# Performance work log

Hardware: AMD Instinct MI355X
Metric: run time of the kernel (lower is better)

## Reference

```python
import jax, jax.numpy as jnp
import numpy as np

T, B, IN, H = 256, 128, 512, 1024


def setup_inputs() -> dict:
    key = jax.random.key(0)
    ks = jax.random.split(key, 13)
    s = 1.0 / float(np.sqrt(H))  # torch LSTMCell init: U(-1/sqrt(H), 1/sqrt(H))
    u = lambda k, shp: jax.random.uniform(k, shp, jnp.float32, -s, s)
    return {
        "x": jax.random.normal(ks[0], (T, B, IN), jnp.float32),
        "h0_fwd": jax.random.normal(ks[1], (B, H), jnp.float32),
        "c0_fwd": jax.random.normal(ks[2], (B, H), jnp.float32),
        "h0_rev": jax.random.normal(ks[3], (B, H), jnp.float32),
        "c0_rev": jax.random.normal(ks[4], (B, H), jnp.float32),
        "W_ih_f": u(ks[5], (4 * H, IN)),
        "W_hh_f": u(ks[6], (4 * H, H)),
        "b_ih_f": u(ks[7], (4 * H,)),
        "b_hh_f": u(ks[8], (4 * H,)),
        "W_ih_r": u(ks[9], (4 * H, IN)),
        "W_hh_r": u(ks[10], (4 * H, H)),
        "b_ih_r": u(ks[11], (4 * H,)),
        "b_hh_r": u(ks[12], (4 * H,)),
    }


def _lstm(x, h0, c0, Wih, Whh, bih, bhh, reverse):
    # Precompute the input projection for all timesteps in one big GEMM.
    xp = jnp.einsum('tbi,gi->tbg', x, Wih) + bih + bhh  # [T, B, 4H]

    def step(carry, xg):
        h, c = carry
        gates = xg + h @ Whh.T  # [B, 4H]
        i, f, g, o = jnp.split(gates, 4, axis=-1)  # torch gate order: i, f, g, o
        c = jax.nn.sigmoid(f) * c + jax.nn.sigmoid(i) * jnp.tanh(g)
        h = jax.nn.sigmoid(o) * jnp.tanh(c)
        return (h, c), h

    # reverse=True scans backward in time but emits outputs in original order,
    # exactly matching ReverseLSTMLayer's reverse-process-then-reverse-outputs.
    (h, c), ys = jax.lax.scan(step, (h0, c0), xp, reverse=reverse)
    return ys, h, c


def reference(x, h0_fwd, c0_fwd, h0_rev, c0_rev,
              W_ih_f, W_hh_f, b_ih_f, b_hh_f,
              W_ih_r, W_hh_r, b_ih_r, b_hh_r):
    yf, hf, cf = _lstm(x, h0_fwd, c0_fwd, W_ih_f, W_hh_f, b_ih_f, b_hh_f, False)
    yr, hr, cr = _lstm(x, h0_rev, c0_rev, W_ih_r, W_hh_r, b_ih_r, b_hh_r, True)
    out = jnp.concatenate([yf, yr], axis=-1)  # [T, B, 2H]
    # Faithful to the original's `hidden, cell = output_states` quirk:
    # `hidden` is the forward direction's (h, c) pair stacked,
    # `cell` is the reverse direction's (h, c) pair stacked.
    hidden = jnp.stack([hf, cf])  # [2, B, H]
    cell = jnp.stack([hr, cr])    # [2, B, H]
    return out, (hidden, cell)
```

## Files before the change

kernel.cpp:

```cpp
#include <hip/hip_runtime.h>
#include <hip/hip_bf16.h>

typedef unsigned short u16;
typedef __attribute__((ext_vector_type(8))) short bf16x8;
typedef __attribute__((ext_vector_type(8))) u16   u16x8;
typedef __attribute__((ext_vector_type(4))) float f32x4;

#define T_STEPS 256
#define BATCH   128
#define INDIM   512
#define HDIM    1024
#define GDIM    4096
#define KTOT    1536

#define OFF_XBF   ((size_t)0)
#define XBF_BYTES ((size_t)T_STEPS * BATCH * INDIM * 2)
#define OFF_BM    (OFF_XBF + XBF_BYTES)
#define BM_BYTES  ((size_t)2 * GDIM * KTOT * 2)
#define OFF_BIAS  (OFF_BM + BM_BYTES)
#define BIAS_BYTES ((size_t)2 * GDIM * 4)
#define OFF_CNT   (OFF_BIAS + BIAS_BYTES)
#define OFF_ROLL  (OFF_CNT + 8192)
#define ROLL_BYTES ((size_t)(T_STEPS + 1) * 2 * BATCH * HDIM * 2)
#define WS_NEED   (OFF_ROLL + ROLL_BYTES)

__device__ __forceinline__ u16 f2b(float f) {
  __hip_bfloat16 h = __float2bfloat16(f);
  return *reinterpret_cast<u16*>(&h);
}

__device__ __forceinline__ void glds16(const void* g, void* l) {
  __builtin_amdgcn_global_load_lds(
      (const __attribute__((address_space(1))) unsigned int*)g,
      (__attribute__((address_space(3))) unsigned int*)l, 16, 0, 0);
}

__global__ void k_cast_x(const float* __restrict__ x, u16* __restrict__ xb) {
  size_t i = ((size_t)blockIdx.x * 256 + threadIdx.x) * 8;
  f32x4 a = *reinterpret_cast<const f32x4*>(x + i);
  f32x4 b = *reinterpret_cast<const f32x4*>(x + i + 4);
  u16x8 u;
  u[0] = f2b(a[0]); u[1] = f2b(a[1]); u[2] = f2b(a[2]); u[3] = f2b(a[3]);
  u[4] = f2b(b[0]); u[5] = f2b(b[1]); u[6] = f2b(b[2]); u[7] = f2b(b[3]);
  *reinterpret_cast<u16x8*>(xb + i) = u;
}

__global__ void k_build_b(const float* __restrict__ Whh_f, const float* __restrict__ Wih_f,
                          const float* __restrict__ Whh_r, const float* __restrict__ Wih_r,
                          u16* __restrict__ Bm) {
  int blk = blockIdx.x;
  int dir = blk >> 6, jt = blk & 63;
  const float* Whh = dir ? Whh_r : Whh_f;
  const float* Wih = dir ? Wih_r : Wih_f;
  u16* dst = Bm + (size_t)blk * 64 * KTOT;
  for (int c = 0; c < 64; c++) {
    int G = (c >> 4) * HDIM + jt * 16 + (c & 15);
    for (int k = threadIdx.x; k < KTOT; k += 256) {
      float v = (k < HDIM) ? Whh[(size_t)G * HDIM + k] : Wih[(size_t)G * INDIM + (k - HDIM)];
      dst[c * KTOT + k] = f2b(v);
    }
  }
}

__global__ void k_init(const float* __restrict__ h0f, const float* __restrict__ h0r,
                       const float* __restrict__ bihf, const float* __restrict__ bhhf,
                       const float* __restrict__ bihr, const float* __restrict__ bhhr,
                       u16* __restrict__ hroll, float* __restrict__ bias,
                       unsigned* __restrict__ flags) {
  int i = blockIdx.x * 256 + threadIdx.x;
  if (i < 2 * BATCH * HDIM) {
    int dir = i / (BATCH * HDIM);
    int rem = i - dir * BATCH * HDIM;
    int r = rem / HDIM, c = rem - r * HDIM;
    const float* h0 = dir ? h0r : h0f;
    char* hb = (char*)hroll;
    *(u16*)(hb + ((size_t)dir * BATCH + r) * 2048 + ((2 * c) ^ ((r & 7) << 4))) =
        f2b(h0[rem]);
  }
  if (i < 2 * GDIM) {
    int dir = i / GDIM, g = i - dir * GDIM;
    bias[i] = dir ? (bihr[g] + bhhr[g]) : (bihf[g] + bhhf[g]);
  }
  if (i < 512) flags[i] = 0;
}

__global__ __launch_bounds__(512, 2) void k_lstm(
    const u16* __restrict__ xb, const u16* __restrict__ Bm,
    u16* __restrict__ hroll,
    const float* __restrict__ bias, unsigned* __restrict__ flags,
    const float* __restrict__ c0f, const float* __restrict__ c0r,
    float* __restrict__ out) {
  __shared__ float ldsf[8 * 64 * 68];
  char* ldsc = reinterpret_cast<char*>(ldsf);

  __builtin_amdgcn_fence(__ATOMIC_ACQUIRE, "agent");

  const int wg   = blockIdx.x;
  const int xcd  = wg & 7, local = wg >> 3;
  const int grp  = xcd >> 1;
  const int dir  = grp >> 1, mt = grp & 1;
  const int jt   = ((xcd & 1) << 5) | local;
  const int tid = threadIdx.x;
  const int w = tid >> 6, lane = tid & 63;
  const int kk = (lane >> 4) * 8;
  const int ar = lane & 15;

  const u16* bsrc = Bm + (size_t)(dir * 64 + jt) * 64 * KTOT;
  bf16x8 bh[4][4];
#pragma unroll
  for (int ks = 0; ks < 4; ks++)
#pragma unroll
    for (int ni = 0; ni < 4; ni++)
      bh[ks][ni] = *reinterpret_cast<const bf16x8*>(
          bsrc + (size_t)(ni * 16 + ar) * KTOT + 128 * w + 32 * ks + kk);

  const int rrow = tid >> 3;
  const int cp   = tid & 7;
  const int jl0  = 2 * cp;
  const int row0 = mt * 64 + rrow;
  const int jg0  = jt * 16 + jl0;
  const float* c0 = dir ? c0r : c0f;
  float2 cc = *reinterpret_cast<const float2*>(c0 + (size_t)row0 * HDIM + jg0);
  float cst0 = cc.x, cst1 = cc.y;
  const float2 b_i = *reinterpret_cast<const float2*>(bias + dir * GDIM + 0 * HDIM + jg0);
  const float2 b_f = *reinterpret_cast<const float2*>(bias + dir * GDIM + 1 * HDIM + jg0);
  const float2 b_g = *reinterpret_cast<const float2*>(bias + dir * GDIM + 2 * HDIM + jg0);
  const float2 b_o = *reinterpret_cast<const float2*>(bias + dir * GDIM + 3 * HDIM + jg0);

  const unsigned* fpA = flags + grp * 64 + lane;

#pragma unroll 1
  for (int s = 0; s < T_STEPS; s++) {
    const int t = dir ? (T_STEPS - 1 - s) : s;

    bf16x8 axm[2][4], bxn[2][4];
    {
      const u16* xsrc = xb + ((size_t)t * BATCH + mt * 64) * INDIM;
#pragma unroll
      for (int ks = 0; ks < 2; ks++) {
#pragma unroll
        for (int mi = 0; mi < 4; mi++)
          axm[ks][mi] = *reinterpret_cast<const bf16x8*>(
              xsrc + (size_t)(16 * mi + ar) * INDIM + 64 * w + 32 * ks + kk);
#pragma unroll
        for (int ni = 0; ni < 4; ni++)
          bxn[ks][ni] = *reinterpret_cast<const bf16x8*>(
              bsrc + (size_t)(ni * 16 + ar) * KTOT + HDIM + 64 * w + 32 * ks + kk);
      }
    }

    if (s > 0) {
      while (true) {
        unsigned f = __hip_atomic_load(fpA, __ATOMIC_RELAXED, __HIP_MEMORY_SCOPE_AGENT);
        if (__all((int)(f >= (unsigned)s))) break;
        __builtin_amdgcn_s_sleep(1);
      }
      __builtin_amdgcn_sched_barrier(0);
    }

    {
      const char* hRd = (const char*)(hroll + ((size_t)s * 2 + dir) * BATCH * HDIM
                                            + (size_t)mt * 64 * HDIM);
      unsigned off = (unsigned)w * 1024 + (unsigned)(lane * 16);
#pragma unroll
      for (int i = 0; i < 16; i++)
        glds16(hRd + off + i * 8192, ldsc + off + i * 8192);
    }

    f32x4 acc[4][4];
#pragma unroll
    for (int mi = 0; mi < 4; mi++)
#pragma unroll
      for (int ni = 0; ni < 4; ni++) acc[mi][ni] = f32x4{0.f, 0.f, 0.f, 0.f};
#pragma unroll
    for (int ks = 0; ks < 2; ks++)
#pragma unroll
      for (int mi = 0; mi < 4; mi++)
#pragma unroll
        for (int ni = 0; ni < 4; ni++)
          acc[mi][ni] = __builtin_amdgcn_mfma_f32_16x16x32_bf16(axm[ks][mi], bxn[ks][ni], acc[mi][ni], 0, 0, 0);

    __syncthreads();

#pragma unroll
    for (int ks = 0; ks < 4; ks++)
#pragma unroll
      for (int mi = 0; mi < 4; mi++) {
        unsigned row = 16 * mi + ar;
        unsigned cb = (128 * w + 32 * ks + kk) * 2;
        bf16x8 af = *reinterpret_cast<const bf16x8*>(
            ldsc + row * 2048 + (cb ^ ((row & 7) << 4)));
#pragma unroll
        for (int ni = 0; ni < 4; ni++)
          acc[mi][ni] = __builtin_amdgcn_mfma_f32_16x16x32_bf16(af, bh[ks][ni], acc[mi][ni], 0, 0, 0);
      }
    __syncthreads();

    {
      float* pw = ldsf + w * (64 * 68);
#pragma unroll
      for (int mi = 0; mi < 4; mi++)
#pragma unroll
        for (int ni = 0; ni < 4; ni++)
          *reinterpret_cast<f32x4*>(pw + (ni * 16 + ar) * 68 + mi * 16 + (lane >> 4) * 4) = acc[mi][ni];
    }
    __syncthreads();

    float h0v, h1v;
    {
      float gi0 = b_i.x, gi1 = b_i.y, gf0 = b_f.x, gf1 = b_f.y;
      float gg0 = b_g.x, gg1 = b_g.y, go0 = b_o.x, go1 = b_o.y;
#pragma unroll
      for (int ww = 0; ww < 8; ww++) {
        const float* p = ldsf + ww * (64 * 68);
        gi0 += p[(0 * 16 + jl0) * 68 + rrow]; gi1 += p[(0 * 16 + jl0 + 1) * 68 + rrow];
        gf0 += p[(1 * 16 + jl0) * 68 + rrow]; gf1 += p[(1 * 16 + jl0 + 1) * 68 + rrow];
        gg0 += p[(2 * 16 + jl0) * 68 + rrow]; gg1 += p[(2 * 16 + jl0 + 1) * 68 + rrow];
        go0 += p[(3 * 16 + jl0) * 68 + rrow]; go1 += p[(3 * 16 + jl0 + 1) * 68 + rrow];
      }
      float i0 = 1.f / (1.f + __expf(-gi0)), i1 = 1.f / (1.f + __expf(-gi1));
      float f0 = 1.f / (1.f + __expf(-gf0)), f1 = 1.f / (1.f + __expf(-gf1));
      float g0 = tanhf(gg0), g1 = tanhf(gg1);
      float o0 = 1.f / (1.f + __expf(-go0)), o1 = 1.f / (1.f + __expf(-go1));
      cst0 = f0 * cst0 + i0 * g0;
      cst1 = f1 * cst1 + i1 * g1;
      h0v = o0 * tanhf(cst0);
      h1v = o1 * tanhf(cst1);

      unsigned hp = (unsigned)f2b(h0v) | ((unsigned)f2b(h1v) << 16);
      char* hb = (char*)(hroll + ((size_t)(s + 1) * 2 + dir) * BATCH * HDIM);
      __hip_atomic_store(
          (unsigned*)(hb + (size_t)row0 * 2048 + ((2 * jg0) ^ ((row0 & 7) << 4))),
          hp, __ATOMIC_RELAXED, __HIP_MEMORY_SCOPE_AGENT);
    }

    asm volatile("s_waitcnt vmcnt(0)" ::: "memory");
    __syncthreads();
    if (tid == 0)
      __hip_atomic_store(flags + grp * 64 + jt, (unsigned)(s + 1),
                         __ATOMIC_RELAXED, __HIP_MEMORY_SCOPE_AGENT);

    {
      float2 yv; yv.x = h0v; yv.y = h1v;
      *reinterpret_cast<float2*>(out + ((size_t)t * BATCH + row0) * (2 * HDIM)
                                     + (size_t)dir * HDIM + jg0) = yv;
      if (s == T_STEPS - 1) {
        size_t hid = (size_t)T_STEPS * BATCH * 2 * HDIM;
        size_t base2 = hid + (size_t)dir * 2 * BATCH * HDIM;
        *reinterpret_cast<float2*>(out + base2 + (size_t)row0 * HDIM + jg0) = yv;
        float2 cv; cv.x = cst0; cv.y = cst1;
        *reinterpret_cast<float2*>(out + base2 + (size_t)BATCH * HDIM
                                       + (size_t)row0 * HDIM + jg0) = cv;
      }
    }
  }
}

extern "C" void kernel_launch(void* const* d_in, const int* in_sizes, int n_in,
                              void* d_out, int out_size, void* d_ws, size_t ws_size,
                              hipStream_t stream) {
  const float* x     = (const float*)d_in[0];
  const float* h0f   = (const float*)d_in[1];
  const float* c0f   = (const float*)d_in[2];
  const float* h0r   = (const float*)d_in[3];
  const float* c0r   = (const float*)d_in[4];
  const float* Wih_f = (const float*)d_in[5];
  const float* Whh_f = (const float*)d_in[6];
  const float* bih_f = (const float*)d_in[7];
  const float* bhh_f = (const float*)d_in[8];
  const float* Wih_r = (const float*)d_in[9];
  const float* Whh_r = (const float*)d_in[10];
  const float* bih_r = (const float*)d_in[11];
  const float* bhh_r = (const float*)d_in[12];
  float* out = (float*)d_out;
  char* ws = (char*)d_ws;

  if (ws_size < WS_NEED) return;

  u16* xbf        = (u16*)(ws + OFF_XBF);
  u16* Bm         = (u16*)(ws + OFF_BM);
  float* bias     = (float*)(ws + OFF_BIAS);
  unsigned* flags = (unsigned*)(ws + OFF_CNT);
  u16* hroll      = (u16*)(ws + OFF_ROLL);

  k_cast_x<<<8192, 256, 0, stream>>>(x, xbf);
  k_build_b<<<128, 256, 0, stream>>>(Whh_f, Wih_f, Whh_r, Wih_r, Bm);
  k_init<<<1024, 256, 0, stream>>>(h0f, h0r, bih_f, bhh_f, bih_r, bhh_r,
                                   hroll, bias, flags);
  k_lstm<<<256, 512, 0, stream>>>(xbf, Bm, hroll, bias, flags, c0f, c0r, out);
}
```

Baseline: 2.038 ms.

## Retile persistent LSTM to 32-row x 128-gate tiles with pre-swizzled x

Each workgroup now owns 32 batch rows by 32 hidden units (128 gate columns) instead of 64 rows by 16 units. Waves split K into four quarters and N into two halves, keeping all recurrent and input weights in registers. This halves the per-step h tile copied into LDS and shrinks the cross-wave reduction from 8 to 4 partials. x is pre-swizzled into MFMA fragment order so each lane does contiguous loads, and the redundant per-step reload of input weights is gone. The trade-off is much higher register pressure from holding 48 weight fragments per lane, plus a changed flag/XCD grouping that may alter which workgroups wait on each other.

```diff
diff --git a/kernel.cpp b/kernel.cpp
--- a/kernel.cpp
+++ b/kernel.cpp
@@ -35,26 +35,37 @@
       (__attribute__((address_space(3))) unsigned int*)l, 16, 0, 0);
 }
 
-__global__ void k_cast_x(const float* __restrict__ x, u16* __restrict__ xb) {
-  size_t i = ((size_t)blockIdx.x * 256 + threadIdx.x) * 8;
-  f32x4 a = *reinterpret_cast<const f32x4*>(x + i);
-  f32x4 b = *reinterpret_cast<const f32x4*>(x + i + 4);
+__global__ void k_cast_x(const float* __restrict__ x, u16* __restrict__ xs) {
+  int i = blockIdx.x * 256 + threadIdx.x;
+  int t   = i >> 13;
+  int r13 = i & 8191;
+  int row = r13 >> 6;
+  int c0  = (r13 & 63) * 8;
+  int q = row >> 5, rloc = row & 31;
+  int mi = rloc >> 4, ar = rloc & 15;
+  int kq = c0 >> 7, kr = c0 & 127;
+  int ks = kr >> 5, h4 = (kr & 31) >> 3;
+  int lane = h4 * 16 + ar;
+  const float* src = x + ((size_t)t * BATCH + row) * INDIM + c0;
+  f32x4 a = *reinterpret_cast<const f32x4*>(src);
+  f32x4 b = *reinterpret_cast<const f32x4*>(src + 4);
   u16x8 u;
   u[0] = f2b(a[0]); u[1] = f2b(a[1]); u[2] = f2b(a[2]); u[3] = f2b(a[3]);
   u[4] = f2b(b[0]); u[5] = f2b(b[1]); u[6] = f2b(b[2]); u[7] = f2b(b[3]);
-  *reinterpret_cast<u16x8*>(xb + i) = u;
+  size_t dst = ((((((size_t)t * 4 + q) * 4 + kq) * 4 + ks) * 2 + mi) * 64 + lane) * 8;
+  *reinterpret_cast<u16x8*>(xs + dst) = u;
 }
 
 __global__ void k_build_b(const float* __restrict__ Whh_f, const float* __restrict__ Wih_f,
                           const float* __restrict__ Whh_r, const float* __restrict__ Wih_r,
                           u16* __restrict__ Bm) {
   int blk = blockIdx.x;
-  int dir = blk >> 6, jt = blk & 63;
+  int dir = blk >> 5, jt = blk & 31;
   const float* Whh = dir ? Whh_r : Whh_f;
   const float* Wih = dir ? Wih_r : Wih_f;
-  u16* dst = Bm + (size_t)blk * 64 * KTOT;
-  for (int c = 0; c < 64; c++) {
-    int G = (c >> 4) * HDIM + jt * 16 + (c & 15);
+  u16* dst = Bm + (size_t)blk * 128 * KTOT;
+  for (int c = 0; c < 128; c++) {
+    int G = (c >> 5) * HDIM + jt * 32 + (c & 31);
     for (int k = threadIdx.x; k < KTOT; k += 256) {
       float v = (k < HDIM) ? Whh[(size_t)G * HDIM + k] : Wih[(size_t)G * INDIM + (k - HDIM)];
       dst[c * KTOT + k] = f2b(v);
@@ -85,40 +96,46 @@
 }
 
 __global__ __launch_bounds__(512, 2) void k_lstm(
-    const u16* __restrict__ xb, const u16* __restrict__ Bm,
+    const u16* __restrict__ xs, const u16* __restrict__ Bm,
     u16* __restrict__ hroll,
     const float* __restrict__ bias, unsigned* __restrict__ flags,
     const float* __restrict__ c0f, const float* __restrict__ c0r,
     float* __restrict__ out) {
-  __shared__ float ldsf[8 * 64 * 68];
+  __shared__ float ldsf[34816];
   char* ldsc = reinterpret_cast<char*>(ldsf);
+  float* ldsP = ldsf + 16384;
 
   __builtin_amdgcn_fence(__ATOMIC_ACQUIRE, "agent");
 
   const int wg   = blockIdx.x;
-  const int xcd  = wg & 7, local = wg >> 3;
-  const int grp  = xcd >> 1;
-  const int dir  = grp >> 1, mt = grp & 1;
-  const int jt   = ((xcd & 1) << 5) | local;
-  const int tid = threadIdx.x;
+  const int grp  = wg & 7;
+  const int dir  = grp >> 2, q = grp & 3;
+  const int jt32 = wg >> 3;
+  const int tid  = threadIdx.x;
   const int w = tid >> 6, lane = tid & 63;
-  const int kk = (lane >> 4) * 8;
+  const int kq = w >> 1, nh = w & 1;
+  const int h4 = lane >> 4, kk = h4 * 8;
   const int ar = lane & 15;
 
-  const u16* bsrc = Bm + (size_t)(dir * 64 + jt) * 64 * KTOT;
-  bf16x8 bh[4][4];
-#pragma unroll
-  for (int ks = 0; ks < 4; ks++)
+  const u16* bsrc = Bm + (size_t)(dir * 32 + jt32) * 128 * KTOT;
+  bf16x8 bh[8][4], bx[4][4];
+#pragma unroll
+  for (int ks = 0; ks < 8; ks++)
 #pragma unroll
     for (int ni = 0; ni < 4; ni++)
       bh[ks][ni] = *reinterpret_cast<const bf16x8*>(
-          bsrc + (size_t)(ni * 16 + ar) * KTOT + 128 * w + 32 * ks + kk);
-
-  const int rrow = tid >> 3;
-  const int cp   = tid & 7;
-  const int jl0  = 2 * cp;
-  const int row0 = mt * 64 + rrow;
-  const int jg0  = jt * 16 + jl0;
+          bsrc + (size_t)(nh * 64 + ni * 16 + ar) * KTOT + 256 * kq + 32 * ks + kk);
+#pragma unroll
+  for (int ks = 0; ks < 4; ks++)
+#pragma unroll
+    for (int ni = 0; ni < 4; ni++)
+      bx[ks][ni] = *reinterpret_cast<const bf16x8*>(
+          bsrc + (size_t)(nh * 64 + ni * 16 + ar) * KTOT + HDIM + 128 * kq + 32 * ks + kk);
+
+  const int rrow = tid & 31;
+  const int jl0  = 2 * (tid >> 5);
+  const int row0 = q * 32 + rrow;
+  const int jg0  = jt32 * 32 + jl0;
   const float* c0 = dir ? c0r : c0f;
   float2 cc = *reinterpret_cast<const float2*>(c0 + (size_t)row0 * HDIM + jg0);
   float cst0 = cc.x, cst1 = cc.y;
@@ -127,26 +144,21 @@
   const float2 b_g = *reinterpret_cast<const float2*>(bias + dir * GDIM + 2 * HDIM + jg0);
   const float2 b_o = *reinterpret_cast<const float2*>(bias + dir * GDIM + 3 * HDIM + jg0);
 
-  const unsigned* fpA = flags + grp * 64 + lane;
+  const unsigned* fpA = flags + grp * 32 + (lane & 31);
 
 #pragma unroll 1
   for (int s = 0; s < T_STEPS; s++) {
     const int t = dir ? (T_STEPS - 1 - s) : s;
 
-    bf16x8 axm[2][4], bxn[2][4];
-    {
-      const u16* xsrc = xb + ((size_t)t * BATCH + mt * 64) * INDIM;
-#pragma unroll
-      for (int ks = 0; ks < 2; ks++) {
-#pragma unroll
-        for (int mi = 0; mi < 4; mi++)
-          axm[ks][mi] = *reinterpret_cast<const bf16x8*>(
-              xsrc + (size_t)(16 * mi + ar) * INDIM + 64 * w + 32 * ks + kk);
-#pragma unroll
-        for (int ni = 0; ni < 4; ni++)
-          bxn[ks][ni] = *reinterpret_cast<const bf16x8*>(
-              bsrc + (size_t)(ni * 16 + ar) * KTOT + HDIM + 64 * w + 32 * ks + kk);
-      }
+    bf16x8 ax[4][2];
+    {
+      const u16* xb = xs + ((((size_t)t * 4 + q) * 4 + kq) * 4) * 2 * 512;
+#pragma unroll
+      for (int ks = 0; ks < 4; ks++)
+#pragma unroll
+        for (int mi = 0; mi < 2; mi++)
+          ax[ks][mi] = *reinterpret_cast<const bf16x8*>(
+              xb + ((size_t)(ks * 2 + mi) * 64 + lane) * 8);
     }
 
     if (s > 0) {
@@ -159,50 +171,56 @@
     }
 
     {
-      const char* hRd = (const char*)(hroll + ((size_t)s * 2 + dir) * BATCH * HDIM
-                                            + (size_t)mt * 64 * HDIM);
-      unsigned off = (unsigned)w * 1024 + (unsigned)(lane * 16);
-#pragma unroll
-      for (int i = 0; i < 16; i++)
+      const char* hRd = (const char*)hroll + ((size_t)s * 2 + dir) * (BATCH * 2048)
+                        + (size_t)q * 32 * 2048;
+      unsigned off = (unsigned)tid * 16;
+#pragma unroll
+      for (int i = 0; i < 8; i++)
         glds16(hRd + off + i * 8192, ldsc + off + i * 8192);
     }
-
-    f32x4 acc[4][4];
-#pragma unroll
-    for (int mi = 0; mi < 4; mi++)
+    __builtin_amdgcn_sched_barrier(0);
+
+    f32x4 acc[2][4];
+#pragma unroll
+    for (int mi = 0; mi < 2; mi++)
 #pragma unroll
       for (int ni = 0; ni < 4; ni++) acc[mi][ni] = f32x4{0.f, 0.f, 0.f, 0.f};
 #pragma unroll
-    for (int ks = 0; ks < 2; ks++)
-#pragma unroll
-      for (int mi = 0; mi < 4; mi++)
+    for (int ks = 0; ks < 4; ks++)
+#pragma unroll
+      for (int mi = 0; mi < 2; mi++)
 #pragma unroll
         for (int ni = 0; ni < 4; ni++)
-          acc[mi][ni] = __builtin_amdgcn_mfma_f32_16x16x32_bf16(axm[ks][mi], bxn[ks][ni], acc[mi][ni], 0, 0, 0);
+          acc[mi][ni] = __builtin_amdgcn_mfma_f32_16x16x32_bf16(ax[ks][mi], bx[ks][ni], acc[mi][ni], 0, 0, 0);
 
     __syncthreads();
 
 #pragma unroll
-    for (int ks = 0; ks < 4; ks++)
-#pragma unroll
-      for (int mi = 0; mi < 4; mi++) {
+    for (int ks = 0; ks < 8; ks++) {
+      bf16x8 af[2];
+#pragma unroll
+      for (int mi = 0; mi < 2; mi++) {
         unsigned row = 16 * mi + ar;
-        unsigned cb = (128 * w + 32 * ks + kk) * 2;
-        bf16x8 af = *reinterpret_cast<const bf16x8*>(
+        unsigned cb = (256 * kq + 32 * ks + kk) * 2;
+        af[mi] = *reinterpret_cast<const bf16x8*>(
             ldsc + row * 2048 + (cb ^ ((row & 7) << 4)));
+      }
+#pragma unroll
+      for (int mi = 0; mi < 2; mi++)
 #pragma unroll
         for (int ni = 0; ni < 4; ni++)
-          acc[mi][ni] = __builtin_amdgcn_mfma_f32_16x16x32_bf16(af, bh[ks][ni], acc[mi][ni], 0, 0, 0);
-      }
-    __syncthreads();
-
-    {
-      float* pw = ldsf + w * (64 * 68);
-#pragma unroll
-      for (int mi = 0; mi < 4; mi++)
-#pragma unroll
-        for (int ni = 0; ni < 4; ni++)
-          *reinterpret_cast<f32x4*>(pw + (ni * 16 + ar) * 68 + mi * 16 + (lane >> 4) * 4) = acc[mi][ni];
+          acc[mi][ni] = __builtin_amdgcn_mfma_f32_16x16x32_bf16(af[mi], bh[ks][ni], acc[mi][ni], 0, 0, 0);
+    }
+
+    {
+      float* pw = ldsP + kq * (128 * 36);
+#pragma unroll
+      for (int mi = 0; mi < 2; mi++)
+#pragma unroll
+        for (int ni = 0; ni < 4; ni++) {
+          int col = nh * 64 + ni * 16 + ar;
+          *reinterpret_cast<f32x4*>(pw + col * 36 + mi * 16 + h4 * 4) = acc[mi][ni];
+        }
     }
     __syncthreads();
 
@@ -211,12 +229,12 @@
       float gi0 = b_i.x, gi1 = b_i.y, gf0 = b_f.x, gf1 = b_f.y;
       float gg0 = b_g.x, gg1 = b_g.y, go0 = b_o.x, go1 = b_o.y;
 #pragma unroll
-      for (int ww = 0; ww < 8; ww++) {
-        const float* p = ldsf + ww * (64 * 68);
-        gi0 += p[(0 * 16 + jl0) * 68 + rrow]; gi1 += p[(0 * 16 + jl0 + 1) * 68 + rrow];
-        gf0 += p[(1 * 16 + jl0) * 68 + rrow]; gf1 += p[(1 * 16 + jl0 + 1) * 68 + rrow];
-        gg0 += p[(2 * 16 + jl0) * 68 + rrow]; gg1 += p[(2 * 16 + jl0 + 1) * 68 + rrow];
-        go0 += p[(3 * 16 + jl0) * 68 + rrow]; go1 += p[(3 * 16 + jl0 + 1) * 68 + rrow];
+      for (int k4 = 0; k4 < 4; k4++) {
+        const float* p = ldsP + k4 * (128 * 36);
+        gi0 += p[(0 * 32 + jl0) * 36 + rrow]; gi1 += p[(0 * 32 + jl0 + 1) * 36 + rrow];
+        gf0 += p[(1 * 32 + jl0) * 36 + rrow]; gf1 += p[(1 * 32 + jl0 + 1) * 36 + rrow];
+        gg0 += p[(2 * 32 + jl0) * 36 + rrow]; gg1 += p[(2 * 32 + jl0 + 1) * 36 + rrow];
+        go0 += p[(3 * 32 + jl0) * 36 + rrow]; go1 += p[(3 * 32 + jl0 + 1) * 36 + rrow];
       }
       float i0 = 1.f / (1.f + __expf(-gi0)), i1 = 1.f / (1.f + __expf(-gi1));
       float f0 = 1.f / (1.f + __expf(-gf0)), f1 = 1.f / (1.f + __expf(-gf1));
@@ -228,7 +246,7 @@
       h1v = o1 * tanhf(cst1);
 
       unsigned hp = (unsigned)f2b(h0v) | ((unsigned)f2b(h1v) << 16);
-      char* hb = (char*)(hroll + ((size_t)(s + 1) * 2 + dir) * BATCH * HDIM);
+      char* hb = (char*)hroll + ((size_t)(s + 1) * 2 + dir) * (BATCH * 2048);
       __hip_atomic_store(
           (unsigned*)(hb + (size_t)row0 * 2048 + ((2 * jg0) ^ ((row0 & 7) << 4))),
           hp, __ATOMIC_RELAXED, __HIP_MEMORY_SCOPE_AGENT);
@@ -237,7 +255,7 @@
     asm volatile("s_waitcnt vmcnt(0)" ::: "memory");
     __syncthreads();
     if (tid == 0)
-      __hip_atomic_store(flags + grp * 64 + jt, (unsigned)(s + 1),
+      __hip_atomic_store(flags + grp * 32 + jt32, (unsigned)(s + 1),
                          __ATOMIC_RELAXED, __HIP_MEMORY_SCOPE_AGENT);
 
     {
@@ -277,15 +295,15 @@
 
   if (ws_size < WS_NEED) return;
 
-  u16* xbf        = (u16*)(ws + OFF_XBF);
+  u16* xsf        = (u16*)(ws + OFF_XBF);
   u16* Bm         = (u16*)(ws + OFF_BM);
   float* bias     = (float*)(ws + OFF_BIAS);
   unsigned* flags = (unsigned*)(ws + OFF_CNT);
   u16* hroll      = (u16*)(ws + OFF_ROLL);
 
-  k_cast_x<<<8192, 256, 0, stream>>>(x, xbf);
-  k_build_b<<<128, 256, 0, stream>>>(Whh_f, Wih_f, Whh_r, Wih_r, Bm);
+  k_cast_x<<<8192, 256, 0, stream>>>(x, xsf);
+  k_build_b<<<64, 256, 0, stream>>>(Whh_f, Wih_f, Whh_r, Wih_r, Bm);
   k_init<<<1024, 256, 0, stream>>>(h0f, h0r, bih_f, bhh_f, bih_r, bhh_r,
                                    hroll, bias, flags);
-  k_lstm<<<256, 512, 0, stream>>>(xbf, Bm, hroll, bias, flags, c0f, c0r, out);
-}
+  k_lstm<<<256, 512, 0, stream>>>(xsf, Bm, hroll, bias, flags, c0f, c0r, out);
+}
```

After: 2.292 ms. 12.4% more time.

## Give each wave a private LDS slice for h and drop two block barriers

Applied to the files above, without the earlier changes.

Each wave now loads only the 128-column K slice of the hidden state it consumes into its own private LDS region. It waits with vmcnt(0) instead of a block-wide barrier. The partial-sum store reuses that private region with an XOR swizzle in place of padding, which removes the barrier between the MFMA phase and the reduction store. This shortens the per-timestep critical path in the latency-bound recurrence, at the cost of a 128KB LDS footprint and relying on wave-private ownership for correctness.

```diff
diff --git a/kernel.cpp b/kernel.cpp
--- a/kernel.cpp
+++ b/kernel.cpp
@@ -90,8 +90,8 @@
     const float* __restrict__ bias, unsigned* __restrict__ flags,
     const float* __restrict__ c0f, const float* __restrict__ c0r,
     float* __restrict__ out) {
-  __shared__ float ldsf[8 * 64 * 68];
-  char* ldsc = reinterpret_cast<char*>(ldsf);
+  __shared__ char ldsc[131072];
+  float* ldsF = reinterpret_cast<float*>(ldsc);
 
   __builtin_amdgcn_fence(__ATOMIC_ACQUIRE, "agent");
 
@@ -102,7 +102,7 @@
   const int jt   = ((xcd & 1) << 5) | local;
   const int tid = threadIdx.x;
   const int w = tid >> 6, lane = tid & 63;
-  const int kk = (lane >> 4) * 8;
+  const int h4 = lane >> 4, kk = h4 * 8;
   const int ar = lane & 15;
 
   const u16* bsrc = Bm + (size_t)(dir * 64 + jt) * 64 * KTOT;
@@ -127,6 +127,9 @@
   const float2 b_g = *reinterpret_cast<const float2*>(bias + dir * GDIM + 2 * HDIM + jg0);
   const float2 b_o = *reinterpret_cast<const float2*>(bias + dir * GDIM + 3 * HDIM + jg0);
 
+  const int xr0 = rrow ^ ((jl0 & 7) << 2);
+  const int xr1 = rrow ^ (((jl0 + 1) & 7) << 2);
+
   const unsigned* fpA = flags + grp * 64 + lane;
 
 #pragma unroll 1
@@ -161,10 +164,12 @@
     {
       const char* hRd = (const char*)(hroll + ((size_t)s * 2 + dir) * BATCH * HDIM
                                             + (size_t)mt * 64 * HDIM);
-      unsigned off = (unsigned)w * 1024 + (unsigned)(lane * 16);
-#pragma unroll
-      for (int i = 0; i < 16; i++)
-        glds16(hRd + off + i * 8192, ldsc + off + i * 8192);
+#pragma unroll
+      for (int i = 0; i < 16; i++) {
+        int r = i * 4 + (lane >> 4);
+        glds16(hRd + (size_t)r * 2048 + 256 * w + (lane & 15) * 16,
+               ldsc + w * 16384 + i * 1024 + lane * 16);
+      }
     }
 
     f32x4 acc[4][4];
@@ -180,29 +185,32 @@
         for (int ni = 0; ni < 4; ni++)
           acc[mi][ni] = __builtin_amdgcn_mfma_f32_16x16x32_bf16(axm[ks][mi], bxn[ks][ni], acc[mi][ni], 0, 0, 0);
 
-    __syncthreads();
+    asm volatile("s_waitcnt vmcnt(0)" ::: "memory");
+    __builtin_amdgcn_sched_barrier(0);
 
 #pragma unroll
     for (int ks = 0; ks < 4; ks++)
 #pragma unroll
       for (int mi = 0; mi < 4; mi++) {
         unsigned row = 16 * mi + ar;
-        unsigned cb = (128 * w + 32 * ks + kk) * 2;
+        unsigned cbl = (32 * ks + kk) * 2;
         bf16x8 af = *reinterpret_cast<const bf16x8*>(
-            ldsc + row * 2048 + (cb ^ ((row & 7) << 4)));
+            ldsc + w * 16384 + row * 256 + (cbl ^ ((row & 7) << 4)));
 #pragma unroll
         for (int ni = 0; ni < 4; ni++)
           acc[mi][ni] = __builtin_amdgcn_mfma_f32_16x16x32_bf16(af, bh[ks][ni], acc[mi][ni], 0, 0, 0);
       }
-    __syncthreads();
-
-    {
-      float* pw = ldsf + w * (64 * 68);
+
+    {
+      float* pw = ldsF + w * 4096;
 #pragma unroll
       for (int mi = 0; mi < 4; mi++)
 #pragma unroll
-        for (int ni = 0; ni < 4; ni++)
-          *reinterpret_cast<f32x4*>(pw + (ni * 16 + ar) * 68 + mi * 16 + (lane >> 4) * 4) = acc[mi][ni];
+        for (int ni = 0; ni < 4; ni++) {
+          int c = ni * 16 + ar;
+          int r = mi * 16 + h4 * 4;
+          *reinterpret_cast<f32x4*>(pw + c * 64 + (r ^ ((c & 7) << 2))) = acc[mi][ni];
+        }
     }
     __syncthreads();
 
@@ -212,11 +220,11 @@
       float gg0 = b_g.x, gg1 = b_g.y, go0 = b_o.x, go1 = b_o.y;
 #pragma unroll
       for (int ww = 0; ww < 8; ww++) {
-        const float* p = ldsf + ww * (64 * 68);
-        gi0 += p[(0 * 16 + jl0) * 68 + rrow]; gi1 += p[(0 * 16 + jl0 + 1) * 68 + rrow];
-        gf0 += p[(1 * 16 + jl0) * 68 + rrow]; gf1 += p[(1 * 16 + jl0 + 1) * 68 + rrow];
-        gg0 += p[(2 * 16 + jl0) * 68 + rrow]; gg1 += p[(2 * 16 + jl0 + 1) * 68 + rrow];
-        go0 += p[(3 * 16 + jl0) * 68 + rrow]; go1 += p[(3 * 16 + jl0 + 1) * 68 + rrow];
+        const float* p = ldsF + ww * 4096;
+        gi0 += p[(0 * 16 + jl0) * 64 + xr0]; gi1 += p[(0 * 16 + jl0 + 1) * 64 + xr1];
+        gf0 += p[(1 * 16 + jl0) * 64 + xr0]; gf1 += p[(1 * 16 + jl0 + 1) * 64 + xr1];
+        gg0 += p[(2 * 16 + jl0) * 64 + xr0]; gg1 += p[(2 * 16 + jl0 + 1) * 64 + xr1];
+        go0 += p[(3 * 16 + jl0) * 64 + xr0]; go1 += p[(3 * 16 + jl0 + 1) * 64 + xr1];
       }
       float i0 = 1.f / (1.f + __expf(-gi0)), i1 = 1.f / (1.f + __expf(-gi1));
       float f0 = 1.f / (1.f + __expf(-gf0)), f1 = 1.f / (1.f + __expf(-gf1));
```

After: 2.002 ms. About the same (-1.8%).
